# Optimization experiments

Hardware: AMD Instinct MI355X
Metric: run time of the kernel (lower is better)

Reference implementation:

```python
import jax, jax.numpy as jnp
import numpy as np

N = 20000   # nodes
D = 64      # emb_dim
H = 512     # 8 * emb_dim
E = 320000  # edges per graph


def setup_inputs() -> dict:
    key = jax.random.key(0)
    ks = jax.random.split(key, 40)
    i = iter(range(40))
    def nrm(shape, s=0.05):
        return jax.random.normal(ks[next(i)], shape, dtype=jnp.float32) * s
    def edges():
        return jax.random.randint(ks[next(i)], (E,), 0, N, dtype=jnp.int32)
    inp = {}
    inp['k_emb'] = nrm((N, D), 1.0)
    inp['pr_src'] = edges(); inp['pr_dst'] = edges()
    inp['pr_ew'] = jax.random.uniform(ks[next(i)], (E,), dtype=jnp.float32)
    inp['cc_src'] = edges(); inp['cc_dst'] = edges()
    inp['cc_ew'] = jax.random.uniform(ks[next(i)], (E,), dtype=jnp.float32)
    inp['sps_src'] = edges(); inp['sps_dst'] = edges()
    inp['pr_Ws0'] = nrm((D, H)); inp['pr_Wn0'] = nrm((D, H)); inp['pr_b0'] = jnp.zeros((H,), jnp.float32)
    inp['pr_Ws1'] = nrm((H, D)); inp['pr_Wn1'] = nrm((H, D)); inp['pr_b1'] = jnp.zeros((D,), jnp.float32)
    inp['cc_Ws0'] = nrm((D, H)); inp['cc_Wn0'] = nrm((D, H)); inp['cc_b0'] = jnp.zeros((H,), jnp.float32)
    inp['cc_Ws1'] = nrm((H, D)); inp['cc_Wn1'] = nrm((H, D)); inp['cc_b1'] = jnp.zeros((D,), jnp.float32)
    inp['ap_Ws0'] = nrm((D, D)); inp['ap_Wn0'] = nrm((D, D)); inp['ap_b0'] = jnp.zeros((D,), jnp.float32)
    inp['ap_Ws1'] = nrm((D, D)); inp['ap_Wn1'] = nrm((D, D)); inp['ap_b1'] = jnp.zeros((D,), jnp.float32)
    inp['att_W'] = nrm((D, D)); inp['att_b'] = jnp.zeros((D,), jnp.float32)
    return inp


def _sage(x, src, dst, ew, Ws, Wn, b):
    # DGL SAGEConv 'mean': neigh = sum(w_e * h_src) / in_degree; out = x@Ws + neigh@Wn + b
    msg = x[src]                                  # [E, din] gather
    if ew is not None:
        msg = msg * ew[:, None]
    agg = jax.ops.segment_sum(msg, dst, num_segments=N)            # [N, din]
    deg = jax.ops.segment_sum(jnp.ones((msg.shape[0],), x.dtype), dst, num_segments=N)
    agg = agg / jnp.maximum(deg, 1.0)[:, None]
    return x @ Ws + agg @ Wn + b


def reference(k_emb, pr_src, pr_dst, pr_ew, cc_src, cc_dst, cc_ew, sps_src, sps_dst,
              pr_Ws0, pr_Wn0, pr_b0, pr_Ws1, pr_Wn1, pr_b1,
              cc_Ws0, cc_Wn0, cc_b0, cc_Ws1, cc_Wn1, cc_b1,
              ap_Ws0, ap_Wn0, ap_b0, ap_Ws1, ap_Wn1, ap_b1,
              att_W, att_b):
    pr = jax.nn.relu(_sage(k_emb, pr_src, pr_dst, pr_ew, pr_Ws0, pr_Wn0, pr_b0))
    pr = _sage(pr, pr_src, pr_dst, pr_ew, pr_Ws1, pr_Wn1, pr_b1)            # [N, D]
    cc = jax.nn.relu(_sage(k_emb, cc_src, cc_dst, cc_ew, cc_Ws0, cc_Wn0, cc_b0))
    cc = _sage(cc, cc_src, cc_dst, cc_ew, cc_Ws1, cc_Wn1, cc_b1)            # [N, D]
    ap = jax.nn.relu(_sage(k_emb, sps_src, sps_dst, None, ap_Ws0, ap_Wn0, ap_b0))
    ap = _sage(ap, sps_src, sps_dst, None, ap_Ws1, ap_Wn1, ap_b1)           # [N, D]
    # APATT fusion
    z = jnp.stack((pr, cc), axis=1)                      # [N, 2, D]
    proj = jnp.tanh(z @ att_W + att_b)                   # [N, 2, D]
    w = jnp.sum(ap[:, None, :] * proj, axis=-1, keepdims=True).mean(0)  # [2, 1]
    beta = jax.nn.softmax(w, axis=0)                     # [2, 1]
    return (beta * z).sum(axis=1)                        # [N, D]
```

## Files before the change

### kernel.cpp

```cpp
#include <hip/hip_runtime.h>

#define NN 20000
#define NP 20032
#define DD 64
#define HH 512
#define EE 320000
#define ATT_BLOCKS 625
#define BLOCKS_E (EE / 256)

typedef __attribute__((ext_vector_type(8))) short short8;
typedef __attribute__((ext_vector_type(4))) float f32x4;

__device__ __forceinline__ ushort f2bf(float f) {
    union { float f; unsigned u; } v; v.f = f;
    unsigned r = v.u + 0x7FFF + ((v.u >> 16) & 1);
    return (ushort)(r >> 16);
}

__global__ __launch_bounds__(256) void hist3(const int* __restrict__ d0,
                                             const int* __restrict__ d1,
                                             const int* __restrict__ d2,
                                             int* __restrict__ cnt) {
    int g = blockIdx.x / BLOCKS_E;
    int e = (blockIdx.x % BLOCKS_E) * 256 + threadIdx.x;
    const int* d = (g == 0) ? d0 : (g == 1) ? d1 : d2;
    if (e < EE) atomicAdd(&cnt[g * NN + d[e]], 1);
}

__global__ __launch_bounds__(256) void inv_kernel(const int* __restrict__ cnt,
                                                  float* __restrict__ invd, int n) {
    int i = blockIdx.x * blockDim.x + threadIdx.x;
    if (i < n) invd[i] = 1.0f / fmaxf((float)cnt[i], 1.0f);
}

__global__ __launch_bounds__(1024) void scan_kernel(const int* __restrict__ cnt,
                                                    int* __restrict__ rowptr) {
    __shared__ int part[1024];
    int g = blockIdx.x;
    const int* c = cnt + g * NN;
    int* rp = rowptr + g * (NN + 1);
    int tid = threadIdx.x;
    const int CH = (NN + 1023) / 1024;
    int i0 = tid * CH;
    int s = 0;
    for (int i = 0; i < CH; ++i) { int idx = i0 + i; if (idx < NN) s += c[idx]; }
    part[tid] = s;
    __syncthreads();
    for (int off = 1; off < 1024; off <<= 1) {
        int v = (tid >= off) ? part[tid - off] : 0;
        __syncthreads();
        part[tid] += v;
        __syncthreads();
    }
    int run = (tid > 0) ? part[tid - 1] : 0;
    for (int i = 0; i < CH; ++i) {
        int idx = i0 + i;
        if (idx < NN) { rp[idx] = run; run += c[idx]; }
    }
    if (tid == 1023) rp[NN] = part[1023];
}

__global__ __launch_bounds__(256) void bucket3(const int* __restrict__ s0, const int* __restrict__ d0, const float* __restrict__ w0,
                                               const int* __restrict__ s1, const int* __restrict__ d1, const float* __restrict__ w1,
                                               const int* __restrict__ s2, const int* __restrict__ d2,
                                               const int* __restrict__ rowptr,
                                               int* __restrict__ cursor,
                                               int2* __restrict__ edge_s,
                                               int* __restrict__ src_s2) {
    int g = blockIdx.x / BLOCKS_E;
    int e = (blockIdx.x % BLOCKS_E) * 256 + threadIdx.x;
    if (e >= EE) return;
    const int* src = (g == 0) ? s0 : (g == 1) ? s1 : s2;
    const int* dst = (g == 0) ? d0 : (g == 1) ? d1 : d2;
    int d = dst[e];
    int pos = rowptr[g * (NN + 1) + d] + atomicAdd(&cursor[g * NN + d], 1);
    if (g < 2) {
        float w = (g == 0) ? w0[e] : w1[e];
        edge_s[(size_t)g * EE + pos] = make_int2(src[e], __float_as_int(w));
    } else {
        src_s2[pos] = src[e];
    }
}

__global__ __launch_bounds__(256) void pull_cast3(const float* __restrict__ x,
                                                  const int* __restrict__ rowptr,
                                                  const int2* __restrict__ edge_s,
                                                  const int* __restrict__ src_s2,
                                                  const float* __restrict__ invd,
                                                  ushort* __restrict__ aggh) {
    int wid = (blockIdx.x * blockDim.x + threadIdx.x) >> 6;
    int lane = threadIdx.x & 63;
    if (wid >= 3 * NN) return;
    int g = wid / NN, n = wid % NN;
    const int* rp = rowptr + g * (NN + 1);
    int beg = rp[n], end = rp[n + 1];
    float a0 = 0.f, a1 = 0.f, a2 = 0.f, a3 = 0.f;
    int i = beg;
    if (g < 2) {
        const int2* es = edge_s + (size_t)g * EE;
        for (; i + 4 <= end; i += 4) {
            int2 e0 = es[i], e1 = es[i + 1], e2 = es[i + 2], e3 = es[i + 3];
            a0 = fmaf(x[e0.x * DD + lane], __int_as_float(e0.y), a0);
            a1 = fmaf(x[e1.x * DD + lane], __int_as_float(e1.y), a1);
            a2 = fmaf(x[e2.x * DD + lane], __int_as_float(e2.y), a2);
            a3 = fmaf(x[e3.x * DD + lane], __int_as_float(e3.y), a3);
        }
        for (; i < end; ++i) { int2 e0 = es[i]; a0 = fmaf(x[e0.x * DD + lane], __int_as_float(e0.y), a0); }
    } else {
        for (; i + 4 <= end; i += 4) {
            int s0 = src_s2[i], s1 = src_s2[i + 1], s2 = src_s2[i + 2], s3 = src_s2[i + 3];
            a0 += x[s0 * DD + lane];
            a1 += x[s1 * DD + lane];
            a2 += x[s2 * DD + lane];
            a3 += x[s3 * DD + lane];
        }
        for (; i < end; ++i) a0 += x[src_s2[i] * DD + lane];
    }
    float acc = (a0 + a1) + (a2 + a3);
    aggh[((size_t)g * NP + n) * 64 + lane] = f2bf(acc * invd[g * NN + n]);
}

__global__ __launch_bounds__(256) void pull_combine3(const float* __restrict__ xn,
                                                     const int* __restrict__ rowptr,
                                                     const int2* __restrict__ edge_s,
                                                     const int* __restrict__ src_s2,
                                                     const float* __restrict__ invd,
                                                     const float* __restrict__ b_pr,
                                                     const float* __restrict__ b_cc,
                                                     const float* __restrict__ b_ap,
                                                     float* __restrict__ o_pr,
                                                     float* __restrict__ o_cc,
                                                     float* __restrict__ o_ap) {
    int wid = (blockIdx.x * blockDim.x + threadIdx.x) >> 6;
    int lane = threadIdx.x & 63;
    if (wid >= 3 * NN) return;
    int g = wid / NN, n = wid % NN;
    const int* rp = rowptr + g * (NN + 1);
    const float* x = xn + (size_t)g * NN * 64;
    const float* bias = (g == 0) ? b_pr : (g == 1) ? b_cc : b_ap;
    float* out = (g == 0) ? o_pr : (g == 1) ? o_cc : o_ap;
    int beg = rp[n], end = rp[n + 1];
    float a0 = 0.f, a1 = 0.f, a2 = 0.f, a3 = 0.f;
    int i = beg;
    if (g < 2) {
        const int2* es = edge_s + (size_t)g * EE;
        for (; i + 4 <= end; i += 4) {
            int2 e0 = es[i], e1 = es[i + 1], e2 = es[i + 2], e3 = es[i + 3];
            a0 = fmaf(x[e0.x * DD + lane], __int_as_float(e0.y), a0);
            a1 = fmaf(x[e1.x * DD + lane], __int_as_float(e1.y), a1);
            a2 = fmaf(x[e2.x * DD + lane], __int_as_float(e2.y), a2);
            a3 = fmaf(x[e3.x * DD + lane], __int_as_float(e3.y), a3);
        }
        for (; i < end; ++i) { int2 e0 = es[i]; a0 = fmaf(x[e0.x * DD + lane], __int_as_float(e0.y), a0); }
    } else {
        for (; i + 4 <= end; i += 4) {
            int s0 = src_s2[i], s1 = src_s2[i + 1], s2 = src_s2[i + 2], s3 = src_s2[i + 3];
            a0 += x[s0 * DD + lane];
            a1 += x[s1 * DD + lane];
            a2 += x[s2 * DD + lane];
            a3 += x[s3 * DD + lane];
        }
        for (; i < end; ++i) a0 += x[src_s2[i] * DD + lane];
    }
    float acc = (a0 + a1) + (a2 + a3);
    out[n * DD + lane] += acc * invd[g * NN + n] + bias[lane];
}

__global__ __launch_bounds__(256) void pack_all(
    const float* __restrict__ pr_Ws0, const float* __restrict__ pr_Wn0,
    const float* __restrict__ cc_Ws0, const float* __restrict__ cc_Wn0,
    const float* __restrict__ pr_Ws1, const float* __restrict__ pr_Wn1,
    const float* __restrict__ cc_Ws1, const float* __restrict__ cc_Wn1,
    const float* __restrict__ ap_Ws0, const float* __restrict__ ap_Wn0,
    const float* __restrict__ ap_Ws1, const float* __restrict__ ap_Wn1,
    const float* __restrict__ k_emb,
    ushort* __restrict__ W0h_pr, ushort* __restrict__ W0h_cc,
    ushort* __restrict__ W1h_pr, ushort* __restrict__ W1h_cc,
    ushort* __restrict__ W0h_ap, ushort* __restrict__ W1h_ap,
    ushort* __restrict__ xh) {
    int b = blockIdx.x;
    int tid = threadIdx.x;
    if (b < 512) {
        int t = (b & 255) * 256 + tid;
        const float* Ws = (b < 256) ? pr_Ws0 : cc_Ws0;
        const float* Wn = (b < 256) ? pr_Wn0 : cc_Wn0;
        ushort* o = (b < 256) ? W0h_pr : W0h_cc;
        int c = t >> 7, k = t & 127;
        o[t] = f2bf((k < 64) ? Ws[k * 512 + c] : Wn[(k - 64) * 512 + c]);
    } else if (b < 1024) {
        int t = ((b - 512) & 255) * 256 + tid;
        const float* Ws = (b < 768) ? pr_Ws1 : cc_Ws1;
        const float* Wn = (b < 768) ? pr_Wn1 : cc_Wn1;
        ushort* o = (b < 768) ? W1h_pr : W1h_cc;
        int c = t >> 9, k = t & 511;
        o[t] = f2bf((c < 64) ? Ws[k * 64 + c] : Wn[k * 64 + (c - 64)]);
    } else if (b < 1056) {
        int t = (b - 1024) * 256 + tid;
        int c = t >> 7, k = t & 127;
        W0h_ap[t] = f2bf((k < 64) ? ap_Ws0[k * 64 + c] : ap_Wn0[(k - 64) * 64 + c]);
    } else if (b < 1088) {
        int t = (b - 1056) * 256 + tid;
        int c = t >> 6, k = t & 63;
        W1h_ap[t] = f2bf((c < 64) ? ap_Ws1[k * 64 + c] : ap_Wn1[k * 64 + (c - 64)]);
    } else {
        int t = (b - 1088) * 256 + tid;
        if (t < NN * DD) xh[t] = f2bf(k_emb[t]);
    }
}

__global__ __launch_bounds__(512, 4) void fused_sage4(
    const ushort* __restrict__ xh,
    const ushort* __restrict__ aggA,
    const ushort* __restrict__ W0a, const ushort* __restrict__ W1a,
    const ushort* __restrict__ W0b, const ushort* __restrict__ W1b,
    const float* __restrict__ b0a, const float* __restrict__ b0b,
    float* __restrict__ outS0, float* __restrict__ outS1,
    float* __restrict__ xn, int nblk) {
    constexpr int LROW = 136;
    __shared__ ushort Ahs[64 * LROW];
    __shared__ ushort h1s[64 * LROW];
    int br = blockIdx.x / nblk;
    int rb = blockIdx.x % nblk;
    const ushort* W0 = br ? W0b : W0a;
    const ushort* W1 = br ? W1b : W1a;
    const float* b0 = br ? b0b : b0a;
    float* outS = br ? outS1 : outS0;
    float* outX = xn + (size_t)br * NN * 64;
    const ushort* agg = aggA + (size_t)br * NP * 64;
    int row0 = rb * 64;

    int wv = threadIdx.x >> 6;
    int lane = threadIdx.x & 63;
    int lrow = lane & 15;
    int koff = (lane >> 4) * 8;
    int crow = (lane >> 4) * 4;

    {
        int r = threadIdx.x >> 3;
        int seg = threadIdx.x & 7;
        const ushort* src = (seg < 4) ? (xh + (size_t)(row0 + r) * 64 + seg * 16)
                                      : (agg + (size_t)(row0 + r) * 64 + (seg - 4) * 16);
        *(short8*)&Ahs[r * LROW + seg * 16] = *(const short8*)src;
        *(short8*)&Ahs[r * LROW + seg * 16 + 8] = *(const short8*)(src + 8);
    }
    __syncthreads();

    f32x4 C[4] = {};
#pragma unroll
    for (int p = 0; p < 4; ++p) {
        {
            short8 B[4];
#pragma unroll
            for (int kk = 0; kk < 4; ++kk)
                B[kk] = *(const short8*)(W0 + (size_t)(p * 128 + wv * 16 + lrow) * 128 + kk * 32 + koff);
            f32x4 acc[4] = {};
#pragma unroll
            for (int rg = 0; rg < 4; ++rg) {
#pragma unroll
                for (int kk = 0; kk < 4; ++kk) {
                    short8 a = *(const short8*)&Ahs[(rg * 16 + lrow) * LROW + kk * 32 + koff];
                    acc[rg] = __builtin_amdgcn_mfma_f32_16x16x32_bf16(a, B[kk], acc[rg], 0, 0, 0);
                }
            }
            float bb = b0[p * 128 + wv * 16 + lrow];
#pragma unroll
            for (int rg = 0; rg < 4; ++rg) {
#pragma unroll
                for (int r = 0; r < 4; ++r) {
                    float v = fmaxf(acc[rg][r] + bb, 0.0f);
                    h1s[(rg * 16 + crow + r) * LROW + wv * 16 + lrow] = f2bf(v);
                }
            }
        }
        __syncthreads();
        {
            short8 B[4];
#pragma unroll
            for (int kc = 0; kc < 4; ++kc)
                B[kc] = *(const short8*)(W1 + (size_t)(wv * 16 + lrow) * HH + p * 128 + kc * 32 + koff);
#pragma unroll
            for (int rg = 0; rg < 4; ++rg) {
#pragma unroll
                for (int kc = 0; kc < 4; ++kc) {
                    short8 a = *(const short8*)&h1s[(rg * 16 + lrow) * LROW + kc * 32 + koff];
                    C[rg] = __builtin_amdgcn_mfma_f32_16x16x32_bf16(a, B[kc], C[rg], 0, 0, 0);
                }
            }
        }
        __syncthreads();
    }
    int col = wv * 16 + lrow;
    float* o = (col < 64) ? (outS + col) : (outX + (col - 64));
#pragma unroll
    for (int rg = 0; rg < 4; ++rg) {
#pragma unroll
        for (int r = 0; r < 4; ++r) {
            int row = row0 + rg * 16 + crow + r;
            if (row < NN) o[(size_t)row * 64] = C[rg][r];
        }
    }
}

__global__ __launch_bounds__(256, 4) void fused_sage_ap(
    const ushort* __restrict__ xh,
    const ushort* __restrict__ agg,
    const ushort* __restrict__ W0,
    const ushort* __restrict__ W1,
    const float* __restrict__ b0,
    float* __restrict__ outS,
    float* __restrict__ outX) {
    constexpr int LROW = 72;
    __shared__ ushort h1s[16 * LROW];
    int wv = threadIdx.x >> 6;
    int lane = threadIdx.x & 63;
    int lrow = lane & 15;
    int koff = (lane >> 4) * 8;
    int crow = (lane >> 4) * 4;
    int row0 = blockIdx.x * 16;

    {
        const size_t aoff = (size_t)(row0 + lrow) * 64 + koff;
        short8 aF[4];
#pragma unroll
        for (int kk = 0; kk < 2; ++kk) {
            aF[kk]     = *(const short8*)(xh + aoff + kk * 32);
            aF[2 + kk] = *(const short8*)(agg + aoff + kk * 32);
        }
        f32x4 acc = {};
#pragma unroll
        for (int kk = 0; kk < 4; ++kk) {
            short8 b = *(const short8*)(W0 + (size_t)(wv * 16 + lrow) * 128 + kk * 32 + koff);
            acc = __builtin_amdgcn_mfma_f32_16x16x32_bf16(aF[kk], b, acc, 0, 0, 0);
        }
        float bb = b0[wv * 16 + lrow];
#pragma unroll
        for (int r = 0; r < 4; ++r) {
            h1s[(crow + r) * LROW + wv * 16 + lrow] = f2bf(fmaxf(acc[r] + bb, 0.0f));
        }
    }
    __syncthreads();
    {
        f32x4 C2[2] = {};
#pragma unroll
        for (int kc = 0; kc < 2; ++kc) {
            short8 a = *(const short8*)&h1s[lrow * LROW + kc * 32 + koff];
#pragma unroll
            for (int c = 0; c < 2; ++c) {
                short8 b = *(const short8*)(W1 + (size_t)(wv * 32 + c * 16 + lrow) * 64 + kc * 32 + koff);
                C2[c] = __builtin_amdgcn_mfma_f32_16x16x32_bf16(a, b, C2[c], 0, 0, 0);
            }
        }
#pragma unroll
        for (int c = 0; c < 2; ++c) {
            int col = wv * 32 + c * 16 + lrow;
            float* o = (col < 64) ? (outS + col) : (outX + (col - 64));
#pragma unroll
            for (int r = 0; r < 4; ++r) {
                int row = row0 + crow + r;
                if (row < NN) o[(size_t)row * 64] = C2[c][r];
            }
        }
    }
}

__global__ __launch_bounds__(256) void att_stage1(const float* __restrict__ pr,
                                                  const float* __restrict__ cc,
                                                  const float* __restrict__ ap,
                                                  const float* __restrict__ attW,
                                                  const float* __restrict__ attb,
                                                  float2* __restrict__ partial) {
    __shared__ float red[8];
    int lane = threadIdx.x & 63;
    int wv = threadIdx.x >> 6;
    int gw = blockIdx.x * 4 + wv;
    const int nwaves = ATT_BLOCKS * 4;
    float b = attb[lane];
    float c0 = 0.f, c1 = 0.f;
    for (int n = gw; n < NN; n += nwaves) {
        float p0 = 0.f, p1 = 0.f;
        for (int k = 0; k < DD; ++k) {
            float w = attW[k * DD + lane];
            p0 = fmaf(pr[n * DD + k], w, p0);
            p1 = fmaf(cc[n * DD + k], w, p1);
        }
        float a = ap[n * DD + lane];
        c0 += a * tanhf(p0 + b);
        c1 += a * tanhf(p1 + b);
    }
#pragma unroll
    for (int off = 32; off; off >>= 1) {
        c0 += __shfl_xor(c0, off);
        c1 += __shfl_xor(c1, off);
    }
    if (lane == 0) { red[wv * 2] = c0; red[wv * 2 + 1] = c1; }
    __syncthreads();
    if (threadIdx.x == 0) {
        partial[blockIdx.x] = make_float2(red[0] + red[2] + red[4] + red[6],
                                          red[1] + red[3] + red[5] + red[7]);
    }
}

__global__ __launch_bounds__(64) void att_stage2(const float2* __restrict__ partial,
                                                 float* __restrict__ w_acc) {
    int lane = threadIdx.x;
    float s0 = 0.f, s1 = 0.f;
    for (int i = lane; i < ATT_BLOCKS; i += 64) {
        float2 p = partial[i];
        s0 += p.x; s1 += p.y;
    }
#pragma unroll
    for (int off = 32; off; off >>= 1) {
        s0 += __shfl_xor(s0, off);
        s1 += __shfl_xor(s1, off);
    }
    if (lane == 0) { w_acc[0] = s0; w_acc[1] = s1; }
}

__global__ __launch_bounds__(256) void final_kernel(float* __restrict__ pr_out,
                                                    const float* __restrict__ cc,
                                                    const float* __restrict__ w_acc) {
    int t = blockIdx.x * blockDim.x + threadIdx.x;
    if (t >= NN * DD) return;
    float w0 = w_acc[0] * (1.0f / NN);
    float w1 = w_acc[1] * (1.0f / NN);
    float m = fmaxf(w0, w1);
    float e0 = __expf(w0 - m), e1 = __expf(w1 - m);
    float inv = 1.0f / (e0 + e1);
    pr_out[t] = (e0 * pr_out[t] + e1 * cc[t]) * inv;
}

extern "C" void kernel_launch(void* const* d_in, const int* in_sizes, int n_in,
                              void* d_out, int out_size, void* d_ws, size_t ws_size,
                              hipStream_t stream) {
    const float* k_emb  = (const float*)d_in[0];
    const int*   pr_src = (const int*)d_in[1];
    const int*   pr_dst = (const int*)d_in[2];
    const float* pr_ew  = (const float*)d_in[3];
    const int*   cc_src = (const int*)d_in[4];
    const int*   cc_dst = (const int*)d_in[5];
    const float* cc_ew  = (const float*)d_in[6];
    const int*   sps_src = (const int*)d_in[7];
    const int*   sps_dst = (const int*)d_in[8];
    const float* pr_Ws0 = (const float*)d_in[9];
    const float* pr_Wn0 = (const float*)d_in[10];
    const float* pr_b0  = (const float*)d_in[11];
    const float* pr_Ws1 = (const float*)d_in[12];
    const float* pr_Wn1 = (const float*)d_in[13];
    const float* pr_b1  = (const float*)d_in[14];
    const float* cc_Ws0 = (const float*)d_in[15];
    const float* cc_Wn0 = (const float*)d_in[16];
    const float* cc_b0  = (const float*)d_in[17];
    const float* cc_Ws1 = (const float*)d_in[18];
    const float* cc_Wn1 = (const float*)d_in[19];
    const float* cc_b1  = (const float*)d_in[20];
    const float* ap_Ws0 = (const float*)d_in[21];
    const float* ap_Wn0 = (const float*)d_in[22];
    const float* ap_b0  = (const float*)d_in[23];
    const float* ap_Ws1 = (const float*)d_in[24];
    const float* ap_Wn1 = (const float*)d_in[25];
    const float* ap_b1  = (const float*)d_in[26];
    const float* att_W  = (const float*)d_in[27];
    const float* att_b  = (const float*)d_in[28];
    float* out = (float*)d_out;

    char* base = (char*)d_ws;
    size_t off = 0;
    auto alloc = [&](size_t bytes) -> void* {
        void* p = base + off;
        off = (off + bytes + 255) & ~(size_t)255;
        return p;
    };
    float*  invd   = (float*)alloc((size_t)3 * NN * 4);
    int*    cnt    = (int*)alloc((size_t)3 * NN * 4);
    int*    rowptr = (int*)alloc((size_t)3 * (NN + 1) * 4);
    int2*   edge_s = (int2*)alloc((size_t)2 * EE * 8);
    int*    src_s2 = (int*)alloc((size_t)EE * 4);
    float*  w_acc  = (float*)alloc(64);
    float2* att_partial = (float2*)alloc(ATT_BLOCKS * 8);
    float*  xn     = (float*)alloc((size_t)3 * NN * DD * 4);
    float*  out_cc = (float*)alloc((size_t)NN * DD * 4);
    float*  out_ap = (float*)alloc((size_t)NN * DD * 4);
    ushort* xh     = (ushort*)alloc((size_t)NP * DD * 2);
    ushort* aggh   = (ushort*)alloc((size_t)3 * NP * DD * 2);
    ushort* W0h_pr = (ushort*)alloc(512 * 128 * 2);
    ushort* W0h_cc = (ushort*)alloc(512 * 128 * 2);
    ushort* W0h_ap = (ushort*)alloc(64 * 128 * 2);
    ushort* W1h_pr = (ushort*)alloc(128 * 512 * 2);
    ushort* W1h_cc = (ushort*)alloc(128 * 512 * 2);
    ushort* W1h_ap = (ushort*)alloc(128 * 64 * 2);
    float*  out_pr = out;

    const int TB = 256;
    const int blocks_ND = (NN * DD) / TB;
    const int blocks_pull3 = (3 * NN * 64) / TB;
    const int NBLK64 = NP / 64;

    pack_all<<<1088 + blocks_ND, TB, 0, stream>>>(
        pr_Ws0, pr_Wn0, cc_Ws0, cc_Wn0, pr_Ws1, pr_Wn1, cc_Ws1, cc_Wn1,
        ap_Ws0, ap_Wn0, ap_Ws1, ap_Wn1, k_emb,
        W0h_pr, W0h_cc, W1h_pr, W1h_cc, W0h_ap, W1h_ap, xh);

    hipMemsetAsync(cnt, 0, (size_t)3 * NN * 4, stream);
    hist3<<<3 * BLOCKS_E, TB, 0, stream>>>(pr_dst, cc_dst, sps_dst, cnt);
    inv_kernel<<<(3 * NN + TB - 1) / TB, TB, 0, stream>>>(cnt, invd, 3 * NN);
    scan_kernel<<<3, 1024, 0, stream>>>(cnt, rowptr);
    hipMemsetAsync(cnt, 0, (size_t)3 * NN * 4, stream);
    bucket3<<<3 * BLOCKS_E, TB, 0, stream>>>(pr_src, pr_dst, pr_ew,
                                             cc_src, cc_dst, cc_ew,
                                             sps_src, sps_dst,
                                             rowptr, cnt, edge_s, src_s2);

    pull_cast3<<<blocks_pull3, TB, 0, stream>>>(k_emb, rowptr, edge_s, src_s2, invd, aggh);

    fused_sage4<<<2 * NBLK64, 512, 0, stream>>>(
        xh, aggh,
        W0h_pr, W1h_pr, W0h_cc, W1h_cc,
        pr_b0, cc_b0, out_pr, out_cc, xn, NBLK64);
    fused_sage_ap<<<NP / 16, 256, 0, stream>>>(
        xh, aggh + (size_t)2 * NP * 64,
        W0h_ap, W1h_ap, ap_b0, out_ap, xn + (size_t)2 * NN * 64);

    pull_combine3<<<blocks_pull3, TB, 0, stream>>>(xn, rowptr, edge_s, src_s2, invd,
                                                   pr_b1, cc_b1, ap_b1,
                                                   out_pr, out_cc, out_ap);

    att_stage1<<<ATT_BLOCKS, TB, 0, stream>>>(out_pr, out_cc, out_ap, att_W, att_b, att_partial);
    att_stage2<<<1, 64, 0, stream>>>(att_partial, w_acc);
    final_kernel<<<blocks_ND, TB, 0, stream>>>(out_pr, out_cc, w_acc);
}
```

Measured before the change: 303.6 us.

## Two-pass local bucketing of edges and bf16 gather of node features

The single global-atomic scatter that sorts edges by destination is replaced by two passes. A coarse pass groups each 4096-edge chunk into 128-node buckets in shared memory and writes them out contiguously. A fine pass then places edges within each bucket using shared-memory atomics. Separately, both gather kernels now read node features as bf16 (the existing xh, and a new bf16 xnh written by the fused SAGE kernels) instead of fp32, halving the gather bytes. This adds an intermediate buffer and extra kernel launches, and lowers the precision of the second-layer aggregation inputs.

```diff
diff --git a/kernel.cpp b/kernel.cpp
--- a/kernel.cpp
+++ b/kernel.cpp
@@ -7,6 +7,9 @@
 #define EE 320000
 #define ATT_BLOCKS 625
 #define BLOCKS_E (EE / 256)
+#define CB 157
+#define EPB 4096
+#define B1_BLOCKS ((EE + EPB - 1) / EPB)
 
 typedef __attribute__((ext_vector_type(8))) short short8;
 typedef __attribute__((ext_vector_type(4))) float f32x4;
@@ -15,6 +18,10 @@
     union { float f; unsigned u; } v; v.f = f;
     unsigned r = v.u + 0x7FFF + ((v.u >> 16) & 1);
     return (ushort)(r >> 16);
+}
+__device__ __forceinline__ float bf2f(ushort h) {
+    union { unsigned u; float f; } v; v.u = ((unsigned)h) << 16;
+    return v.f;
 }
 
 __global__ __launch_bounds__(256) void hist3(const int* __restrict__ d0,
@@ -60,29 +67,89 @@
     if (tid == 1023) rp[NN] = part[1023];
 }
 
-__global__ __launch_bounds__(256) void bucket3(const int* __restrict__ s0, const int* __restrict__ d0, const float* __restrict__ w0,
-                                               const int* __restrict__ s1, const int* __restrict__ d1, const float* __restrict__ w1,
-                                               const int* __restrict__ s2, const int* __restrict__ d2,
-                                               const int* __restrict__ rowptr,
-                                               int* __restrict__ cursor,
-                                               int2* __restrict__ edge_s,
-                                               int* __restrict__ src_s2) {
-    int g = blockIdx.x / BLOCKS_E;
-    int e = (blockIdx.x % BLOCKS_E) * 256 + threadIdx.x;
-    if (e >= EE) return;
-    const int* src = (g == 0) ? s0 : (g == 1) ? s1 : s2;
-    const int* dst = (g == 0) ? d0 : (g == 1) ? d1 : d2;
-    int d = dst[e];
-    int pos = rowptr[g * (NN + 1) + d] + atomicAdd(&cursor[g * NN + d], 1);
-    if (g < 2) {
-        float w = (g == 0) ? w0[e] : w1[e];
-        edge_s[(size_t)g * EE + pos] = make_int2(src[e], __float_as_int(w));
-    } else {
-        src_s2[pos] = src[e];
-    }
-}
-
-__global__ __launch_bounds__(256) void pull_cast3(const float* __restrict__ x,
+__global__ __launch_bounds__(256) void bucket_coarse(
+    const int* __restrict__ s0, const int* __restrict__ d0, const float* __restrict__ w0,
+    const int* __restrict__ s1, const int* __restrict__ d1, const float* __restrict__ w1,
+    const int* __restrict__ s2, const int* __restrict__ d2,
+    const int* __restrict__ rowptr,
+    int* __restrict__ ccur,
+    int2* __restrict__ ce,
+    ushort* __restrict__ cd) {
+    __shared__ int cnt_s[CB];
+    __shared__ int off_s[CB];
+    __shared__ int pos_s[CB];
+    __shared__ int gbase[CB];
+    __shared__ int lsrc[EPB];
+    __shared__ int lew[EPB];
+    __shared__ ushort ldst[EPB];
+    int g = blockIdx.x / B1_BLOCKS;
+    int blk = blockIdx.x % B1_BLOCKS;
+    const int* S = (g == 0) ? s0 : (g == 1) ? s1 : s2;
+    const int* D = (g == 0) ? d0 : (g == 1) ? d1 : d2;
+    const float* W = (g == 0) ? w0 : (g == 1) ? w1 : nullptr;
+    int e0 = blk * EPB;
+    int n = min(EPB, EE - e0);
+    for (int i = threadIdx.x; i < CB; i += 256) cnt_s[i] = 0;
+    __syncthreads();
+    for (int i = threadIdx.x; i < n; i += 256)
+        atomicAdd(&cnt_s[D[e0 + i] >> 7], 1);
+    __syncthreads();
+    if (threadIdx.x == 0) {
+        int run = 0;
+        for (int i = 0; i < CB; ++i) { off_s[i] = run; run += cnt_s[i]; }
+    }
+    __syncthreads();
+    if (threadIdx.x < CB) pos_s[threadIdx.x] = off_s[threadIdx.x];
+    __syncthreads();
+    for (int i = threadIdx.x; i < n; i += 256) {
+        int e = e0 + i;
+        int d = D[e];
+        int p = atomicAdd(&pos_s[d >> 7], 1);
+        lsrc[p] = S[e];
+        lew[p] = (g < 2) ? __float_as_int(W[e]) : 0;
+        ldst[p] = (ushort)d;
+    }
+    __syncthreads();
+    if (threadIdx.x < CB)
+        gbase[threadIdx.x] = atomicAdd(&ccur[g * CB + threadIdx.x], cnt_s[threadIdx.x]);
+    __syncthreads();
+    const int* rp = rowptr + g * (NN + 1);
+    for (int j = threadIdx.x; j < n; j += 256) {
+        ushort d = ldst[j];
+        int cb = d >> 7;
+        int gpos = rp[cb << 7] + gbase[cb] + (j - off_s[cb]);
+        ce[(size_t)g * EE + gpos] = make_int2(lsrc[j], lew[j]);
+        cd[(size_t)g * EE + gpos] = d;
+    }
+}
+
+__global__ __launch_bounds__(256) void bucket_fine(
+    const int* __restrict__ rowptr,
+    const int2* __restrict__ ce, const ushort* __restrict__ cd,
+    int2* __restrict__ edge_s,
+    int* __restrict__ src_s2) {
+    __shared__ int rp_s[129];
+    __shared__ int cur_s[128];
+    int g = blockIdx.x / CB;
+    int cb = blockIdx.x % CB;
+    const int* rp = rowptr + g * (NN + 1);
+    int n0 = cb << 7;
+    int n1 = min(n0 + 128, NN);
+    int m = n1 - n0;
+    if (threadIdx.x <= m) rp_s[threadIdx.x] = rp[n0 + threadIdx.x];
+    if (threadIdx.x < m) cur_s[threadIdx.x] = 0;
+    __syncthreads();
+    int beg = rp_s[0], end = rp_s[m];
+    for (int j = beg + threadIdx.x; j < end; j += 256) {
+        int2 e = ce[(size_t)g * EE + j];
+        int dl = (int)cd[(size_t)g * EE + j] - n0;
+        int pos = rp_s[dl] + atomicAdd(&cur_s[dl], 1);
+        if (g < 2) edge_s[(size_t)g * EE + pos] = e;
+        else src_s2[pos] = e.x;
+    }
+}
+
+__global__ __launch_bounds__(256) void pull_cast3(const ushort* __restrict__ xh,
                                                   const int* __restrict__ rowptr,
                                                   const int2* __restrict__ edge_s,
                                                   const int* __restrict__ src_s2,
@@ -100,27 +167,27 @@
         const int2* es = edge_s + (size_t)g * EE;
         for (; i + 4 <= end; i += 4) {
             int2 e0 = es[i], e1 = es[i + 1], e2 = es[i + 2], e3 = es[i + 3];
-            a0 = fmaf(x[e0.x * DD + lane], __int_as_float(e0.y), a0);
-            a1 = fmaf(x[e1.x * DD + lane], __int_as_float(e1.y), a1);
-            a2 = fmaf(x[e2.x * DD + lane], __int_as_float(e2.y), a2);
-            a3 = fmaf(x[e3.x * DD + lane], __int_as_float(e3.y), a3);
-        }
-        for (; i < end; ++i) { int2 e0 = es[i]; a0 = fmaf(x[e0.x * DD + lane], __int_as_float(e0.y), a0); }
+            a0 = fmaf(bf2f(xh[e0.x * DD + lane]), __int_as_float(e0.y), a0);
+            a1 = fmaf(bf2f(xh[e1.x * DD + lane]), __int_as_float(e1.y), a1);
+            a2 = fmaf(bf2f(xh[e2.x * DD + lane]), __int_as_float(e2.y), a2);
+            a3 = fmaf(bf2f(xh[e3.x * DD + lane]), __int_as_float(e3.y), a3);
+        }
+        for (; i < end; ++i) { int2 e0 = es[i]; a0 = fmaf(bf2f(xh[e0.x * DD + lane]), __int_as_float(e0.y), a0); }
     } else {
         for (; i + 4 <= end; i += 4) {
             int s0 = src_s2[i], s1 = src_s2[i + 1], s2 = src_s2[i + 2], s3 = src_s2[i + 3];
-            a0 += x[s0 * DD + lane];
-            a1 += x[s1 * DD + lane];
-            a2 += x[s2 * DD + lane];
-            a3 += x[s3 * DD + lane];
-        }
-        for (; i < end; ++i) a0 += x[src_s2[i] * DD + lane];
+            a0 += bf2f(xh[s0 * DD + lane]);
+            a1 += bf2f(xh[s1 * DD + lane]);
+            a2 += bf2f(xh[s2 * DD + lane]);
+            a3 += bf2f(xh[s3 * DD + lane]);
+        }
+        for (; i < end; ++i) a0 += bf2f(xh[src_s2[i] * DD + lane]);
     }
     float acc = (a0 + a1) + (a2 + a3);
     aggh[((size_t)g * NP + n) * 64 + lane] = f2bf(acc * invd[g * NN + n]);
 }
 
-__global__ __launch_bounds__(256) void pull_combine3(const float* __restrict__ xn,
+__global__ __launch_bounds__(256) void pull_combine3(const ushort* __restrict__ xnh,
                                                      const int* __restrict__ rowptr,
                                                      const int2* __restrict__ edge_s,
                                                      const int* __restrict__ src_s2,
@@ -136,7 +203,7 @@
     if (wid >= 3 * NN) return;
     int g = wid / NN, n = wid % NN;
     const int* rp = rowptr + g * (NN + 1);
-    const float* x = xn + (size_t)g * NN * 64;
+    const ushort* x = xnh + (size_t)g * NP * 64;
     const float* bias = (g == 0) ? b_pr : (g == 1) ? b_cc : b_ap;
     float* out = (g == 0) ? o_pr : (g == 1) ? o_cc : o_ap;
     int beg = rp[n], end = rp[n + 1];
@@ -146,21 +213,21 @@
         const int2* es = edge_s + (size_t)g * EE;
         for (; i + 4 <= end; i += 4) {
             int2 e0 = es[i], e1 = es[i + 1], e2 = es[i + 2], e3 = es[i + 3];
-            a0 = fmaf(x[e0.x * DD + lane], __int_as_float(e0.y), a0);
-            a1 = fmaf(x[e1.x * DD + lane], __int_as_float(e1.y), a1);
-            a2 = fmaf(x[e2.x * DD + lane], __int_as_float(e2.y), a2);
-            a3 = fmaf(x[e3.x * DD + lane], __int_as_float(e3.y), a3);
-        }
-        for (; i < end; ++i) { int2 e0 = es[i]; a0 = fmaf(x[e0.x * DD + lane], __int_as_float(e0.y), a0); }
+            a0 = fmaf(bf2f(x[e0.x * DD + lane]), __int_as_float(e0.y), a0);
+            a1 = fmaf(bf2f(x[e1.x * DD + lane]), __int_as_float(e1.y), a1);
+            a2 = fmaf(bf2f(x[e2.x * DD + lane]), __int_as_float(e2.y), a2);
+            a3 = fmaf(bf2f(x[e3.x * DD + lane]), __int_as_float(e3.y), a3);
+        }
+        for (; i < end; ++i) { int2 e0 = es[i]; a0 = fmaf(bf2f(x[e0.x * DD + lane]), __int_as_float(e0.y), a0); }
     } else {
         for (; i + 4 <= end; i += 4) {
             int s0 = src_s2[i], s1 = src_s2[i + 1], s2 = src_s2[i + 2], s3 = src_s2[i + 3];
-            a0 += x[s0 * DD + lane];
-            a1 += x[s1 * DD + lane];
-            a2 += x[s2 * DD + lane];
-            a3 += x[s3 * DD + lane];
-        }
-        for (; i < end; ++i) a0 += x[src_s2[i] * DD + lane];
+            a0 += bf2f(x[s0 * DD + lane]);
+            a1 += bf2f(x[s1 * DD + lane]);
+            a2 += bf2f(x[s2 * DD + lane]);
+            a3 += bf2f(x[s3 * DD + lane]);
+        }
+        for (; i < end; ++i) a0 += bf2f(x[src_s2[i] * DD + lane]);
     }
     float acc = (a0 + a1) + (a2 + a3);
     out[n * DD + lane] += acc * invd[g * NN + n] + bias[lane];
@@ -215,7 +282,7 @@
     const ushort* __restrict__ W0b, const ushort* __restrict__ W1b,
     const float* __restrict__ b0a, const float* __restrict__ b0b,
     float* __restrict__ outS0, float* __restrict__ outS1,
-    float* __restrict__ xn, int nblk) {
+    ushort* __restrict__ xnh, int nblk) {
     constexpr int LROW = 136;
     __shared__ ushort Ahs[64 * LROW];
     __shared__ ushort h1s[64 * LROW];
@@ -225,7 +292,7 @@
     const ushort* W1 = br ? W1b : W1a;
     const float* b0 = br ? b0b : b0a;
     float* outS = br ? outS1 : outS0;
-    float* outX = xn + (size_t)br * NN * 64;
+    ushort* outX = xnh + (size_t)br * NP * 64;
     const ushort* agg = aggA + (size_t)br * NP * 64;
     int row0 = rb * 64;
 
@@ -290,14 +357,24 @@
         __syncthreads();
     }
     int col = wv * 16 + lrow;
-    float* o = (col < 64) ? (outS + col) : (outX + (col - 64));
-#pragma unroll
-    for (int rg = 0; rg < 4; ++rg) {
-#pragma unroll
-        for (int r = 0; r < 4; ++r) {
-            int row = row0 + rg * 16 + crow + r;
-            if (row < NN) o[(size_t)row * 64] = C[rg][r];
-        }
+    if (col < 64) {
+        float* o = outS + col;
+#pragma unroll
+        for (int rg = 0; rg < 4; ++rg)
+#pragma unroll
+            for (int r = 0; r < 4; ++r) {
+                int row = row0 + rg * 16 + crow + r;
+                if (row < NN) o[(size_t)row * 64] = C[rg][r];
+            }
+    } else {
+        ushort* o = outX + (col - 64);
+#pragma unroll
+        for (int rg = 0; rg < 4; ++rg)
+#pragma unroll
+            for (int r = 0; r < 4; ++r) {
+                int row = row0 + rg * 16 + crow + r;
+                if (row < NN) o[(size_t)row * 64] = f2bf(C[rg][r]);
+            }
     }
 }
 
@@ -308,7 +385,7 @@
     const ushort* __restrict__ W1,
     const float* __restrict__ b0,
     float* __restrict__ outS,
-    float* __restrict__ outX) {
+    ushort* __restrict__ outX) {
     constexpr int LROW = 72;
     __shared__ ushort h1s[16 * LROW];
     int wv = threadIdx.x >> 6;
@@ -353,11 +430,13 @@
 #pragma unroll
         for (int c = 0; c < 2; ++c) {
             int col = wv * 32 + c * 16 + lrow;
-            float* o = (col < 64) ? (outS + col) : (outX + (col - 64));
 #pragma unroll
             for (int r = 0; r < 4; ++r) {
                 int row = row0 + crow + r;
-                if (row < NN) o[(size_t)row * 64] = C2[c][r];
+                if (row < NN) {
+                    if (col < 64) outS[(size_t)row * 64 + col] = C2[c][r];
+                    else outX[(size_t)row * 64 + (col - 64)] = f2bf(C2[c][r]);
+                }
             }
         }
     }
@@ -471,13 +550,16 @@
         return p;
     };
     float*  invd   = (float*)alloc((size_t)3 * NN * 4);
-    int*    cnt    = (int*)alloc((size_t)3 * NN * 4);
+    int*    cnt    = (int*)alloc((size_t)(3 * NN + 3 * CB) * 4);
+    int*    ccur   = cnt + 3 * NN;
     int*    rowptr = (int*)alloc((size_t)3 * (NN + 1) * 4);
     int2*   edge_s = (int2*)alloc((size_t)2 * EE * 8);
     int*    src_s2 = (int*)alloc((size_t)EE * 4);
+    int2*   ce     = (int2*)alloc((size_t)3 * EE * 8);
+    ushort* cd     = (ushort*)alloc((size_t)3 * EE * 2);
     float*  w_acc  = (float*)alloc(64);
     float2* att_partial = (float2*)alloc(ATT_BLOCKS * 8);
-    float*  xn     = (float*)alloc((size_t)3 * NN * DD * 4);
+    ushort* xnh    = (ushort*)alloc((size_t)3 * NP * DD * 2);
     float*  out_cc = (float*)alloc((size_t)NN * DD * 4);
     float*  out_ap = (float*)alloc((size_t)NN * DD * 4);
     ushort* xh     = (ushort*)alloc((size_t)NP * DD * 2);
@@ -500,27 +582,27 @@
         ap_Ws0, ap_Wn0, ap_Ws1, ap_Wn1, k_emb,
         W0h_pr, W0h_cc, W1h_pr, W1h_cc, W0h_ap, W1h_ap, xh);
 
-    hipMemsetAsync(cnt, 0, (size_t)3 * NN * 4, stream);
+    hipMemsetAsync(cnt, 0, (size_t)(3 * NN + 3 * CB) * 4, stream);
     hist3<<<3 * BLOCKS_E, TB, 0, stream>>>(pr_dst, cc_dst, sps_dst, cnt);
     inv_kernel<<<(3 * NN + TB - 1) / TB, TB, 0, stream>>>(cnt, invd, 3 * NN);
     scan_kernel<<<3, 1024, 0, stream>>>(cnt, rowptr);
-    hipMemsetAsync(cnt, 0, (size_t)3 * NN * 4, stream);
-    bucket3<<<3 * BLOCKS_E, TB, 0, stream>>>(pr_src, pr_dst, pr_ew,
-                                             cc_src, cc_dst, cc_ew,
-                                             sps_src, sps_dst,
-                                             rowptr, cnt, edge_s, src_s2);
-
-    pull_cast3<<<blocks_pull3, TB, 0, stream>>>(k_emb, rowptr, edge_s, src_s2, invd, aggh);
+    bucket_coarse<<<3 * B1_BLOCKS, TB, 0, stream>>>(pr_src, pr_dst, pr_ew,
+                                                    cc_src, cc_dst, cc_ew,
+                                                    sps_src, sps_dst,
+                                                    rowptr, ccur, ce, cd);
+    bucket_fine<<<3 * CB, TB, 0, stream>>>(rowptr, ce, cd, edge_s, src_s2);
+
+    pull_cast3<<<blocks_pull3, TB, 0, stream>>>(xh, rowptr, edge_s, src_s2, invd, aggh);
 
     fused_sage4<<<2 * NBLK64, 512, 0, stream>>>(
         xh, aggh,
         W0h_pr, W1h_pr, W0h_cc, W1h_cc,
-        pr_b0, cc_b0, out_pr, out_cc, xn, NBLK64);
+        pr_b0, cc_b0, out_pr, out_cc, xnh, NBLK64);
     fused_sage_ap<<<NP / 16, 256, 0, stream>>>(
         xh, aggh + (size_t)2 * NP * 64,
-        W0h_ap, W1h_ap, ap_b0, out_ap, xn + (size_t)2 * NN * 64);
-
-    pull_combine3<<<blocks_pull3, TB, 0, stream>>>(xn, rowptr, edge_s, src_s2, invd,
+        W0h_ap, W1h_ap, ap_b0, out_ap, xnh + (size_t)2 * NP * 64);
+
+    pull_combine3<<<blocks_pull3, TB, 0, stream>>>(xnh, rowptr, edge_s, src_s2, invd,
                                                    pr_b1, cc_b1, ap_b1,
                                                    out_pr, out_cc, out_ap);
 
```

Measured after the change: 278.8 us. 8.2% less time.
